# Kernel optimization log

Hardware: AMD Instinct MI355X
Metric: run time of the kernel (lower is better)

## Reference

```python
import jax, jax.numpy as jnp
import numpy as np

N_HEAD = 16
LN_EPS = 1e-5

def setup_inputs() -> dict:
    key = jax.random.key(0)
    ks = jax.random.split(key, 8)
    Lq, Lk, B, D = 1024, 1024, 8, 1024
    std = np.sqrt(2.0 / (D + D)).astype(np.float32)  # reset_parameters std
    return {
        "q": jax.random.normal(ks[0], (Lq, B, D), jnp.float32),
        "k": jax.random.normal(ks[1], (Lk, B, D), jnp.float32),
        "mask": jnp.zeros((B, Lk), jnp.bool_),
        "Wq": jax.random.normal(ks[2], (D, D), jnp.float32) * std,
        "Wkv": jax.random.normal(ks[3], (2 * D, D), jnp.float32) * std,
        "Wo": jax.random.normal(ks[4], (D, D), jnp.float32) * std,
        "ln_g": jnp.ones((D,), jnp.float32),
        "ln_b": jnp.zeros((D,), jnp.float32),
    }

def reference(q, k, mask, Wq, Wkv, Wo, ln_g, ln_b):
    Lq, B, D = q.shape
    Lk = k.shape[0]
    H = N_HEAD
    dk = D // H
    scaling = dk ** -0.5

    residual = q
    # LayerNorm over last dim
    mu = jnp.mean(q, axis=-1, keepdims=True)
    var = jnp.mean(jnp.square(q - mu), axis=-1, keepdims=True)
    qn = (q - mu) * jax.lax.rsqrt(var + LN_EPS) * ln_g + ln_b

    # fused projections (no bias)
    Q = (qn @ Wq.T) * scaling                      # [Lq,B,D]
    KV = k @ Wkv.T                                 # [Lk,B,2D]
    K, V = KV[..., :D], KV[..., D:]

    Qh = Q.reshape(Lq, B, H, dk)
    Kh = K.reshape(Lk, B, H, dk)
    Vh = V.reshape(Lk, B, H, dk)

    scores = jnp.einsum('qbhd,kbhd->bhqk', Qh, Kh)  # [B,H,Lq,Lk]
    scores = jnp.where(mask[:, None, None, :], jnp.float32(-1e9), scores)
    attn = jax.nn.softmax(scores, axis=-1)          # coverage [B,H,Lq,Lk]

    ctx = jnp.einsum('bhqk,kbhd->qbhd', attn, Vh).reshape(Lq, B, D)
    out = ctx @ Wo.T  # scale=1.0
    out = out + residual
    return out, attn
```

## Files before the change

### kernel.cpp

```cpp
#include <hip/hip_runtime.h>
#include <stdint.h>

typedef __bf16 bf16x8 __attribute__((ext_vector_type(8)));
typedef float f32x4 __attribute__((ext_vector_type(4)));

#define LQ 1024
#define LK 1024
#define BB 8
#define DD 1024
#define HH 16
#define DK 64

__device__ __forceinline__ unsigned short f2bf(float f) {
  union { float f; unsigned u; } v; v.f = f;
  unsigned u = v.u;
  u += 0x7FFFu + ((u >> 16) & 1u);
  return (unsigned short)(u >> 16);
}
__device__ __forceinline__ float bf2f(unsigned short u) {
  union { unsigned u; float f; } v; v.u = ((unsigned)u) << 16;
  return v.f;
}
__device__ __forceinline__ f32x4 mfma16(bf16x8 a, bf16x8 b, f32x4 c) {
  return __builtin_amdgcn_mfma_f32_16x16x32_bf16(a, b, c, 0, 0, 0);
}
__device__ __forceinline__ void gload_lds16(const unsigned short* g, unsigned short* l) {
  __builtin_amdgcn_global_load_lds(
      (const __attribute__((address_space(1))) void*)g,
      (__attribute__((address_space(3))) void*)l, 16, 0, 0);
}

__global__ __launch_bounds__(256) void cvt_k(const float* __restrict__ in,
                                             unsigned short* __restrict__ out,
                                             int n4) {
  int i = blockIdx.x * 256 + threadIdx.x;
  if (i < n4) {
    float4 v = *(const float4*)(in + (size_t)i * 4);
    uint2 o;
    o.x = f2bf(v.x) | ((unsigned)f2bf(v.y) << 16);
    o.y = f2bf(v.z) | ((unsigned)f2bf(v.w) << 16);
    *(uint2*)(out + (size_t)i * 4) = o;
  }
}

__global__ __launch_bounds__(256) void cvtW_k(const float* __restrict__ Wq,
                                              const float* __restrict__ Wkv,
                                              const float* __restrict__ Wo,
                                              unsigned short* __restrict__ oq,
                                              unsigned short* __restrict__ okv,
                                              unsigned short* __restrict__ oo) {
  int i = blockIdx.x * 256 + threadIdx.x;
  const float* in;
  unsigned short* out;
  int j;
  if (i < 262144) { in = Wq; out = oq; j = i; }
  else if (i < 786432) { in = Wkv; out = okv; j = i - 262144; }
  else { in = Wo; out = oo; j = i - 786432; }
  float4 v = *(const float4*)(in + (size_t)j * 4);
  uint2 o;
  o.x = f2bf(v.x) | ((unsigned)f2bf(v.y) << 16);
  o.y = f2bf(v.z) | ((unsigned)f2bf(v.w) << 16);
  *(uint2*)(out + (size_t)j * 4) = o;
}

__global__ __launch_bounds__(256) void layernorm_k(const float* __restrict__ x,
                                                   const float* __restrict__ g,
                                                   const float* __restrict__ bta,
                                                   unsigned short* __restrict__ out) {
  const int row = blockIdx.x;
  const float* xr = x + (size_t)row * DD;
  const int t = threadIdx.x;
  float4 v = *(const float4*)(xr + t * 4);
  float s = v.x + v.y + v.z + v.w;
  float s2 = v.x * v.x + v.y * v.y + v.z * v.z + v.w * v.w;
  for (int off = 32; off > 0; off >>= 1) {
    s += __shfl_down(s, off);
    s2 += __shfl_down(s2, off);
  }
  __shared__ float red[8];
  int lane = t & 63, w = t >> 6;
  if (lane == 0) { red[w] = s; red[4 + w] = s2; }
  __syncthreads();
  s = red[0] + red[1] + red[2] + red[3];
  s2 = red[4] + red[5] + red[6] + red[7];
  float mu = s * (1.0f / 1024.0f);
  float var = s2 * (1.0f / 1024.0f) - mu * mu;
  float inv = rsqrtf(var + 1e-5f);
  float4 gv = *(const float4*)(g + t * 4);
  float4 bv = *(const float4*)(bta + t * 4);
  uint2 o;
  o.x = f2bf((v.x - mu) * inv * gv.x + bv.x) |
        ((unsigned)f2bf((v.y - mu) * inv * gv.y + bv.y) << 16);
  o.y = f2bf((v.z - mu) * inv * gv.z + bv.z) |
        ((unsigned)f2bf((v.w - mu) * inv * gv.w + bv.w) << 16);
  *(uint2*)(out + (size_t)row * DD + t * 4) = o;
}

template <bool OUT_F32, bool ADD_RES>
__global__ __launch_bounds__(256) void gemm_bt_k(const unsigned short* __restrict__ A, int lda,
                                                 const unsigned short* __restrict__ B, int ldb,
                                                 void* __restrict__ Cv, int ldc,
                                                 const float* __restrict__ res,
                                                 float scale, int K) {
  __shared__ __align__(16) unsigned short As[128 * 64];
  __shared__ __align__(16) unsigned short Bs[128 * 64];
  const int t = threadIdx.x;
  const int lane = t & 63, wave = t >> 6;
  const int fr = lane & 15, fq = lane >> 4;
  const int wr = (wave >> 1) * 64, wc = (wave & 1) * 64;
  const int m0 = blockIdx.y * 128, n0 = blockIdx.x * 128;
  const int lrow = lane >> 3, lcol = (lane & 7) * 8;
  f32x4 acc[4][4] = {};
  for (int k0 = 0; k0 < K; k0 += 64) {
    __syncthreads();
#pragma unroll
    for (int i = 0; i < 4; ++i) {
      int rbase = wave * 32 + i * 8;
      int r = rbase + lrow;
      gload_lds16(A + (size_t)(m0 + r) * lda + k0 + lcol, &As[rbase * 64]);
      gload_lds16(B + (size_t)(n0 + r) * ldb + k0 + lcol, &Bs[rbase * 64]);
    }
    __syncthreads();
#pragma unroll
    for (int ks = 0; ks < 2; ++ks) {
      bf16x8 af[4], bb[4];
#pragma unroll
      for (int m = 0; m < 4; ++m)
        af[m] = *(const bf16x8*)&As[(wr + m * 16 + fr) * 64 + ks * 32 + fq * 8];
#pragma unroll
      for (int n = 0; n < 4; ++n)
        bb[n] = *(const bf16x8*)&Bs[(wc + n * 16 + fr) * 64 + ks * 32 + fq * 8];
#pragma unroll
      for (int m = 0; m < 4; ++m)
#pragma unroll
        for (int n = 0; n < 4; ++n)
          acc[m][n] = mfma16(af[m], bb[n], acc[m][n]);
    }
  }
#pragma unroll
  for (int m = 0; m < 4; ++m)
#pragma unroll
    for (int n = 0; n < 4; ++n)
#pragma unroll
      for (int i = 0; i < 4; ++i) {
        int r = m0 + wr + m * 16 + fq * 4 + i;
        int c = n0 + wc + n * 16 + fr;
        float vv = acc[m][n][i] * scale;
        if (OUT_F32) {
          float rs = ADD_RES ? res[(size_t)r * ldc + c] : 0.0f;
          __builtin_nontemporal_store(vv + rs, (float*)Cv + (size_t)r * ldc + c);
        } else {
          ((unsigned short*)Cv)[(size_t)r * ldc + c] = f2bf(vv);
        }
      }
}

__global__ __launch_bounds__(256) void gemm_vt_k(const unsigned short* __restrict__ A, int lda,
                                                 const unsigned short* __restrict__ B, int ldb,
                                                 unsigned short* __restrict__ Vt, int K) {
  __shared__ __align__(16) unsigned short As[128 * 64];
  __shared__ __align__(16) unsigned short Bs[128 * 64];
  const int t = threadIdx.x;
  const int lane = t & 63, wave = t >> 6;
  const int fr = lane & 15, fq = lane >> 4;
  const int wr = (wave >> 1) * 64, wc = (wave & 1) * 64;
  const int m0 = blockIdx.y * 128, n0 = blockIdx.x * 128;
  const int lrow = lane >> 3, lcol = (lane & 7) * 8;
  f32x4 acc[4][4] = {};
  for (int k0 = 0; k0 < K; k0 += 64) {
    __syncthreads();
#pragma unroll
    for (int i = 0; i < 4; ++i) {
      int rbase = wave * 32 + i * 8;
      int r = rbase + lrow;
      gload_lds16(A + (size_t)(m0 + r) * lda + k0 + lcol, &As[rbase * 64]);
      gload_lds16(B + (size_t)(n0 + r) * ldb + k0 + lcol, &Bs[rbase * 64]);
    }
    __syncthreads();
#pragma unroll
    for (int ks = 0; ks < 2; ++ks) {
      bf16x8 af[4], bb[4];
#pragma unroll
      for (int m = 0; m < 4; ++m)
        af[m] = *(const bf16x8*)&As[(wr + m * 16 + fr) * 64 + ks * 32 + fq * 8];
#pragma unroll
      for (int n = 0; n < 4; ++n)
        bb[n] = *(const bf16x8*)&Bs[(wc + n * 16 + fr) * 64 + ks * 32 + fq * 8];
#pragma unroll
      for (int m = 0; m < 4; ++m)
#pragma unroll
        for (int n = 0; n < 4; ++n)
          acc[m][n] = mfma16(af[m], bb[n], acc[m][n]);
    }
  }
#pragma unroll
  for (int m = 0; m < 4; ++m)
#pragma unroll
    for (int n = 0; n < 4; ++n)
#pragma unroll
      for (int i = 0; i < 4; ++i) {
        int r = m0 + wr + m * 16 + fq * 4 + i;
        int c = n0 + wc + n * 16 + fr;
        int kk = r >> 3, b_ = r & 7, h_ = c >> 6, d_ = c & 63;
        Vt[(((size_t)(b_ * 16 + h_) * 64 + d_) << 10) + kk] = f2bf(acc[m][n][i]);
      }
}

__global__ __launch_bounds__(256, 2) void attn_fused_k(
    const unsigned short* __restrict__ Q,
    const unsigned short* __restrict__ K,
    const unsigned short* __restrict__ Vt,
    const unsigned char* __restrict__ mask,
    float* __restrict__ attn,
    unsigned short* __restrict__ ctx) {
  __shared__ __align__(16) unsigned short KVu[128 * 72];
  __shared__ __align__(16) unsigned short Ps[64 * 128];
  __shared__ float lrow[64];
  __shared__ float ps2[64][2], maskv[128];

  const int t = threadIdx.x;
  const int lane = t & 63, wave = t >> 6;
  const int fr = lane & 15, fq = lane >> 4;
  const int L = blockIdx.x;
  const int xcd = L & 7;
  const int idx = L >> 3;
  const int bh = xcd * 16 + (idx >> 4);
  const int qt = idx & 15;
  const int b = bh >> 4, h = bh & 15;
  const int wrk = (wave >> 1) * 64;
  const int wcq = (wave & 1) * 32;
  const int w01 = wave >> 1;
  const int swz = (fr & 7) << 4;

  bf16x8 qf[2][2];
#pragma unroll
  for (int n = 0; n < 2; ++n)
#pragma unroll
    for (int c = 0; c < 2; ++c)
      qf[n][c] = *(const bf16x8*)(Q +
          (((size_t)(qt * 64 + wcq + n * 16 + fr) * 8 + b) << 10) + h * 64 + c * 32 + fq * 8);

  float s_run[2] = {0.0f, 0.0f};
  for (int kt = 0; kt < 8; ++kt) {
    __syncthreads();
#pragma unroll
    for (int it = 0; it < 4; ++it) {
      int idx2 = it * 256 + t;
      int r = idx2 >> 3, c8 = (idx2 & 7) << 3;
      *(uint4*)&KVu[r * 72 + c8] =
          *(const uint4*)(K + (((size_t)(kt * 128 + r) * 8 + b) << 10) + h * 64 + c8);
    }
    if (t < 128) maskv[t] = mask[b * 1024 + kt * 128 + t] ? -1.0e9f : 0.0f;
    __syncthreads();
    f32x4 acc[4][2] = {};
#pragma unroll
    for (int k0 = 0; k0 < 2; ++k0) {
      bf16x8 af[4];
#pragma unroll
      for (int m = 0; m < 4; ++m)
        af[m] = *(const bf16x8*)&KVu[(wrk + m * 16 + fr) * 72 + k0 * 32 + fq * 8];
      __builtin_amdgcn_s_setprio(1);
#pragma unroll
      for (int m = 0; m < 4; ++m)
#pragma unroll
        for (int n = 0; n < 2; ++n)
          acc[m][n] = mfma16(af[m], qf[n][k0], acc[m][n]);
      __builtin_amdgcn_s_setprio(0);
    }
    float4 mk[4];
#pragma unroll
    for (int m = 0; m < 4; ++m) mk[m] = *(const float4*)&maskv[wrk + m * 16 + fq * 4];
#pragma unroll
    for (int n = 0; n < 2; ++n) {
      float s = 0.0f;
#pragma unroll
      for (int m = 0; m < 4; ++m) {
        s += __builtin_amdgcn_exp2f(acc[m][n][0] + mk[m].x);
        s += __builtin_amdgcn_exp2f(acc[m][n][1] + mk[m].y);
        s += __builtin_amdgcn_exp2f(acc[m][n][2] + mk[m].z);
        s += __builtin_amdgcn_exp2f(acc[m][n][3] + mk[m].w);
      }
      s_run[n] += s;
    }
  }
#pragma unroll
  for (int n = 0; n < 2; ++n) {
    float s = s_run[n];
    s += __shfl_xor(s, 16);
    s += __shfl_xor(s, 32);
    if (fq == 0) ps2[wcq + n * 16 + fr][w01] = s;
  }
  __syncthreads();
  if (t < 64) lrow[t] = 1.0f / (ps2[t][0] + ps2[t][1]);

  const int wq = (wave >> 1) * 32, wd = (wave & 1) * 32;
  f32x4 accv[2][2] = {};
  for (int kt = 0; kt < 8; ++kt) {
    __syncthreads();
#pragma unroll
    for (int it = 0; it < 4; ++it) {
      int idx2 = it * 256 + t;
      int r = idx2 >> 3, c8 = (idx2 & 7) << 3;
      *(uint4*)&KVu[r * 72 + c8] =
          *(const uint4*)(K + (((size_t)(kt * 128 + r) * 8 + b) << 10) + h * 64 + c8);
    }
    if (t < 128) maskv[t] = mask[b * 1024 + kt * 128 + t] ? -1.0e9f : 0.0f;
    __syncthreads();
    f32x4 acc[4][2] = {};
#pragma unroll
    for (int k0 = 0; k0 < 2; ++k0) {
      bf16x8 af[4];
#pragma unroll
      for (int m = 0; m < 4; ++m)
        af[m] = *(const bf16x8*)&KVu[(wrk + m * 16 + fr) * 72 + k0 * 32 + fq * 8];
      __builtin_amdgcn_s_setprio(1);
#pragma unroll
      for (int m = 0; m < 4; ++m)
#pragma unroll
        for (int n = 0; n < 2; ++n)
          acc[m][n] = mfma16(af[m], qf[n][k0], acc[m][n]);
      __builtin_amdgcn_s_setprio(0);
    }
    float4 mk[4];
#pragma unroll
    for (int m = 0; m < 4; ++m) mk[m] = *(const float4*)&maskv[wrk + m * 16 + fq * 4];
#pragma unroll
    for (int m = 0; m < 4; ++m)
#pragma unroll
      for (int n = 0; n < 2; ++n) {
        acc[m][n][0] += mk[m].x; acc[m][n][1] += mk[m].y;
        acc[m][n][2] += mk[m].z; acc[m][n][3] += mk[m].w;
      }
    float il[2];
#pragma unroll
    for (int n = 0; n < 2; ++n) il[n] = lrow[wcq + n * 16 + fr];
#pragma unroll
    for (int m = 0; m < 4; ++m) {
      int k4 = wrk + m * 16 + fq * 4;
#pragma unroll
      for (int n = 0; n < 2; ++n) {
        float p0 = __builtin_amdgcn_exp2f(acc[m][n][0]) * il[n];
        float p1 = __builtin_amdgcn_exp2f(acc[m][n][1]) * il[n];
        float p2 = __builtin_amdgcn_exp2f(acc[m][n][2]) * il[n];
        float p3 = __builtin_amdgcn_exp2f(acc[m][n][3]) * il[n];
        uint2 w;
        w.x = f2bf(p0) | ((unsigned)f2bf(p1) << 16);
        w.y = f2bf(p2) | ((unsigned)f2bf(p3) << 16);
        int row = wcq + n * 16 + fr;
        *(uint2*)((char*)Ps + row * 256 + ((k4 * 2) ^ swz)) = w;
      }
    }
    __syncthreads();
#pragma unroll
    for (int it = 0; it < 8; ++it) {
      int idx2 = it * 256 + t;
      int row = idx2 >> 5, colb = (idx2 & 31) << 3;
      uint2 d2 = *(const uint2*)((const char*)Ps + row * 256 + (colb ^ ((row & 7) << 4)));
      f32x4 o;
      o[0] = bf2f((unsigned short)(d2.x & 0xFFFF));
      o[1] = bf2f((unsigned short)(d2.x >> 16));
      o[2] = bf2f((unsigned short)(d2.y & 0xFFFF));
      o[3] = bf2f((unsigned short)(d2.y >> 16));
      __builtin_nontemporal_store(
          o, (f32x4*)(attn + ((size_t)bh * 1024 + qt * 64 + row) * 1024 + kt * 128 + (colb >> 1)));
    }
#pragma unroll
    for (int it = 0; it < 4; ++it) {
      int idx2 = it * 256 + t;
      int dd = idx2 >> 4, k8 = (idx2 & 15) << 3;
      *(uint4*)&KVu[dd * 136 + k8] =
          *(const uint4*)(Vt + (((size_t)(b * 16 + h) * 64 + dd) << 10) + kt * 128 + k8);
    }
    __syncthreads();
#pragma unroll
    for (int ks = 0; ks < 4; ++ks) {
      bf16x8 pa[2], vb[2];
#pragma unroll
      for (int m2 = 0; m2 < 2; ++m2) {
        int row = wq + m2 * 16 + fr;
        pa[m2] = *(const bf16x8*)((const char*)Ps + row * 256 + (((ks * 32 + fq * 8) * 2) ^ swz));
      }
#pragma unroll
      for (int n2 = 0; n2 < 2; ++n2)
        vb[n2] = *(const bf16x8*)&KVu[(wd + n2 * 16 + fr) * 136 + ks * 32 + fq * 8];
      __builtin_amdgcn_s_setprio(1);
#pragma unroll
      for (int m2 = 0; m2 < 2; ++m2)
#pragma unroll
        for (int n2 = 0; n2 < 2; ++n2)
          accv[m2][n2] = mfma16(pa[m2], vb[n2], accv[m2][n2]);
      __builtin_amdgcn_s_setprio(0);
    }
  }
#pragma unroll
  for (int m2 = 0; m2 < 2; ++m2)
#pragma unroll
    for (int n2 = 0; n2 < 2; ++n2)
#pragma unroll
      for (int i = 0; i < 4; ++i) {
        int qrow = qt * 64 + wq + m2 * 16 + fq * 4 + i;
        int c = h * 64 + wd + n2 * 16 + fr;
        ctx[(((size_t)qrow * 8 + b) << 10) + c] = f2bf(accv[m2][n2][i]);
      }
}

extern "C" void kernel_launch(void* const* d_in, const int* in_sizes, int n_in,
                              void* d_out, int out_size, void* d_ws, size_t ws_size,
                              hipStream_t stream) {
  const float* q = (const float*)d_in[0];
  const float* k = (const float*)d_in[1];
  const unsigned char* mask = (const unsigned char*)d_in[2];
  const float* Wq = (const float*)d_in[3];
  const float* Wkv = (const float*)d_in[4];
  const float* Wo = (const float*)d_in[5];
  const float* ln_g = (const float*)d_in[6];
  const float* ln_b = (const float*)d_in[7];

  float* out0 = (float*)d_out;
  float* attn = out0 + (size_t)LQ * BB * DD;

  char* ws = (char*)d_ws;
  unsigned short* qn   = (unsigned short*)(ws);
  unsigned short* kbf  = (unsigned short*)(ws + ((size_t)16 << 20));
  unsigned short* Qw   = (unsigned short*)(ws + ((size_t)32 << 20));
  unsigned short* ctxw = (unsigned short*)(ws + ((size_t)48 << 20));
  unsigned short* Kw   = (unsigned short*)(ws + ((size_t)64 << 20));
  unsigned short* Vtg  = (unsigned short*)(ws + ((size_t)80 << 20));
  unsigned short* Wqb  = (unsigned short*)(ws + ((size_t)96 << 20));
  unsigned short* Wkvb = (unsigned short*)(ws + ((size_t)98 << 20));
  unsigned short* Wob  = (unsigned short*)(ws + ((size_t)102 << 20));

  cvt_k<<<8192, 256, 0, stream>>>(k, kbf, (LK * BB * DD) / 4);
  cvtW_k<<<4096, 256, 0, stream>>>(Wq, Wkv, Wo, Wqb, Wkvb, Wob);

  layernorm_k<<<LQ * BB, 256, 0, stream>>>(q, ln_g, ln_b, qn);

  gemm_bt_k<false, false><<<dim3(8, 64), 256, 0, stream>>>(
      qn, DD, Wqb, DD, Qw, DD, nullptr, 0.18033688011112f, DD);

  gemm_bt_k<false, false><<<dim3(8, 64), 256, 0, stream>>>(
      kbf, DD, Wkvb, DD, Kw, DD, nullptr, 1.0f, DD);

  gemm_vt_k<<<dim3(8, 64), 256, 0, stream>>>(
      kbf, DD, Wkvb + ((size_t)1 << 20), DD, Vtg, DD);

  attn_fused_k<<<dim3(16 * BB * HH), 256, 0, stream>>>(Qw, Kw, Vtg, mask, attn, ctxw);

  gemm_bt_k<true, true><<<dim3(8, 64), 256, 0, stream>>>(
      ctxw, DD, Wob, DD, out0, DD, q, 1.0f, DD);
}
```

Before: 294.0 us.

## Load K fragments directly from global and prefetch V into registers

K tiles are no longer staged through shared memory. Each wave loads its MFMA A-fragments straight from global memory, which removes two barriers per K tile in both passes. Mask bytes are read directly as packed 32-bit words instead of being staged through a shared float array. V is prefetched into registers at the start of each tile and written to a dedicated shared buffer alongside P, saving one barrier per tile and overlapping the V fetch with QK compute. In exchange, K global reads are duplicated across the two waves that share rows, and the prefetch raises register pressure.

```diff
diff --git a/kernel.cpp b/kernel.cpp
--- a/kernel.cpp
+++ b/kernel.cpp
@@ -213,10 +213,10 @@
     const unsigned char* __restrict__ mask,
     float* __restrict__ attn,
     unsigned short* __restrict__ ctx) {
-  __shared__ __align__(16) unsigned short KVu[128 * 72];
+  __shared__ __align__(16) unsigned short Vs[64 * 136];
   __shared__ __align__(16) unsigned short Ps[64 * 128];
   __shared__ float lrow[64];
-  __shared__ float ps2[64][2], maskv[128];
+  __shared__ float ps2[64][2];
 
   const int t = threadIdx.x;
   const int lane = t & 63, wave = t >> 6;
@@ -242,23 +242,14 @@
 
   float s_run[2] = {0.0f, 0.0f};
   for (int kt = 0; kt < 8; ++kt) {
-    __syncthreads();
-#pragma unroll
-    for (int it = 0; it < 4; ++it) {
-      int idx2 = it * 256 + t;
-      int r = idx2 >> 3, c8 = (idx2 & 7) << 3;
-      *(uint4*)&KVu[r * 72 + c8] =
-          *(const uint4*)(K + (((size_t)(kt * 128 + r) * 8 + b) << 10) + h * 64 + c8);
-    }
-    if (t < 128) maskv[t] = mask[b * 1024 + kt * 128 + t] ? -1.0e9f : 0.0f;
-    __syncthreads();
     f32x4 acc[4][2] = {};
 #pragma unroll
     for (int k0 = 0; k0 < 2; ++k0) {
       bf16x8 af[4];
 #pragma unroll
       for (int m = 0; m < 4; ++m)
-        af[m] = *(const bf16x8*)&KVu[(wrk + m * 16 + fr) * 72 + k0 * 32 + fq * 8];
+        af[m] = *(const bf16x8*)(K +
+            (((size_t)(kt * 128 + wrk + m * 16 + fr) * 8 + b) << 10) + h * 64 + k0 * 32 + fq * 8);
       __builtin_amdgcn_s_setprio(1);
 #pragma unroll
       for (int m = 0; m < 4; ++m)
@@ -267,20 +258,21 @@
           acc[m][n] = mfma16(af[m], qf[n][k0], acc[m][n]);
       __builtin_amdgcn_s_setprio(0);
     }
-    float4 mk[4];
-#pragma unroll
-    for (int m = 0; m < 4; ++m) mk[m] = *(const float4*)&maskv[wrk + m * 16 + fq * 4];
-#pragma unroll
-    for (int n = 0; n < 2; ++n) {
-      float s = 0.0f;
-#pragma unroll
-      for (int m = 0; m < 4; ++m) {
-        s += __builtin_amdgcn_exp2f(acc[m][n][0] + mk[m].x);
-        s += __builtin_amdgcn_exp2f(acc[m][n][1] + mk[m].y);
-        s += __builtin_amdgcn_exp2f(acc[m][n][2] + mk[m].z);
-        s += __builtin_amdgcn_exp2f(acc[m][n][3] + mk[m].w);
-      }
-      s_run[n] += s;
+#pragma unroll
+    for (int m = 0; m < 4; ++m) {
+      unsigned mw = *(const unsigned*)(mask + b * 1024 + kt * 128 + wrk + m * 16 + fq * 4);
+      float4 mk;
+      mk.x = (mw & 0xFFu) ? -1.0e9f : 0.0f;
+      mk.y = (mw & 0xFF00u) ? -1.0e9f : 0.0f;
+      mk.z = (mw & 0xFF0000u) ? -1.0e9f : 0.0f;
+      mk.w = (mw & 0xFF000000u) ? -1.0e9f : 0.0f;
+#pragma unroll
+      for (int n = 0; n < 2; ++n) {
+        s_run[n] += __builtin_amdgcn_exp2f(acc[m][n][0] + mk.x);
+        s_run[n] += __builtin_amdgcn_exp2f(acc[m][n][1] + mk.y);
+        s_run[n] += __builtin_amdgcn_exp2f(acc[m][n][2] + mk.z);
+        s_run[n] += __builtin_amdgcn_exp2f(acc[m][n][3] + mk.w);
+      }
     }
   }
 #pragma unroll
@@ -292,27 +284,29 @@
   }
   __syncthreads();
   if (t < 64) lrow[t] = 1.0f / (ps2[t][0] + ps2[t][1]);
+  __syncthreads();
+  float il[2];
+#pragma unroll
+  for (int n = 0; n < 2; ++n) il[n] = lrow[wcq + n * 16 + fr];
 
   const int wq = (wave >> 1) * 32, wd = (wave & 1) * 32;
+  const int vdd = t >> 4, vk8 = (t & 15) << 3;
   f32x4 accv[2][2] = {};
   for (int kt = 0; kt < 8; ++kt) {
-    __syncthreads();
+    uint4 vreg[4];
 #pragma unroll
     for (int it = 0; it < 4; ++it) {
-      int idx2 = it * 256 + t;
-      int r = idx2 >> 3, c8 = (idx2 & 7) << 3;
-      *(uint4*)&KVu[r * 72 + c8] =
-          *(const uint4*)(K + (((size_t)(kt * 128 + r) * 8 + b) << 10) + h * 64 + c8);
-    }
-    if (t < 128) maskv[t] = mask[b * 1024 + kt * 128 + t] ? -1.0e9f : 0.0f;
-    __syncthreads();
+      int dd = (it * 256 + t) >> 4, k8 = ((it * 256 + t) & 15) << 3;
+      vreg[it] = *(const uint4*)(Vt + (((size_t)(b * 16 + h) * 64 + dd) << 10) + kt * 128 + k8);
+    }
     f32x4 acc[4][2] = {};
 #pragma unroll
     for (int k0 = 0; k0 < 2; ++k0) {
       bf16x8 af[4];
 #pragma unroll
       for (int m = 0; m < 4; ++m)
-        af[m] = *(const bf16x8*)&KVu[(wrk + m * 16 + fr) * 72 + k0 * 32 + fq * 8];
+        af[m] = *(const bf16x8*)(K +
+            (((size_t)(kt * 128 + wrk + m * 16 + fr) * 8 + b) << 10) + h * 64 + k0 * 32 + fq * 8);
       __builtin_amdgcn_s_setprio(1);
 #pragma unroll
       for (int m = 0; m < 4; ++m)
@@ -321,19 +315,18 @@
           acc[m][n] = mfma16(af[m], qf[n][k0], acc[m][n]);
       __builtin_amdgcn_s_setprio(0);
     }
-    float4 mk[4];
-#pragma unroll
-    for (int m = 0; m < 4; ++m) mk[m] = *(const float4*)&maskv[wrk + m * 16 + fq * 4];
-#pragma unroll
-    for (int m = 0; m < 4; ++m)
+#pragma unroll
+    for (int m = 0; m < 4; ++m) {
+      unsigned mw = *(const unsigned*)(mask + b * 1024 + kt * 128 + wrk + m * 16 + fq * 4);
 #pragma unroll
       for (int n = 0; n < 2; ++n) {
-        acc[m][n][0] += mk[m].x; acc[m][n][1] += mk[m].y;
-        acc[m][n][2] += mk[m].z; acc[m][n][3] += mk[m].w;
-      }
-    float il[2];
-#pragma unroll
-    for (int n = 0; n < 2; ++n) il[n] = lrow[wcq + n * 16 + fr];
+        acc[m][n][0] += (mw & 0xFFu) ? -1.0e9f : 0.0f;
+        acc[m][n][1] += (mw & 0xFF00u) ? -1.0e9f : 0.0f;
+        acc[m][n][2] += (mw & 0xFF0000u) ? -1.0e9f : 0.0f;
+        acc[m][n][3] += (mw & 0xFF000000u) ? -1.0e9f : 0.0f;
+      }
+    }
+    __syncthreads();
 #pragma unroll
     for (int m = 0; m < 4; ++m) {
       int k4 = wrk + m * 16 + fq * 4;
@@ -349,6 +342,11 @@
         int row = wcq + n * 16 + fr;
         *(uint2*)((char*)Ps + row * 256 + ((k4 * 2) ^ swz)) = w;
       }
+    }
+#pragma unroll
+    for (int it = 0; it < 4; ++it) {
+      int dd = (it * 256 + t) >> 4, k8 = ((it * 256 + t) & 15) << 3;
+      *(uint4*)&Vs[dd * 136 + k8] = vreg[it];
     }
     __syncthreads();
 #pragma unroll
@@ -365,14 +363,6 @@
           o, (f32x4*)(attn + ((size_t)bh * 1024 + qt * 64 + row) * 1024 + kt * 128 + (colb >> 1)));
     }
 #pragma unroll
-    for (int it = 0; it < 4; ++it) {
-      int idx2 = it * 256 + t;
-      int dd = idx2 >> 4, k8 = (idx2 & 15) << 3;
-      *(uint4*)&KVu[dd * 136 + k8] =
-          *(const uint4*)(Vt + (((size_t)(b * 16 + h) * 64 + dd) << 10) + kt * 128 + k8);
-    }
-    __syncthreads();
-#pragma unroll
     for (int ks = 0; ks < 4; ++ks) {
       bf16x8 pa[2], vb[2];
 #pragma unroll
@@ -382,7 +372,7 @@
       }
 #pragma unroll
       for (int n2 = 0; n2 < 2; ++n2)
-        vb[n2] = *(const bf16x8*)&KVu[(wd + n2 * 16 + fr) * 136 + ks * 32 + fq * 8];
+        vb[n2] = *(const bf16x8*)&Vs[(wd + n2 * 16 + fr) * 136 + ks * 32 + fq * 8];
       __builtin_amdgcn_s_setprio(1);
 #pragma unroll
       for (int m2 = 0; m2 < 2; ++m2)
```

Measured after the change: 366.3 us. 24.6% more time.
